# Kernel optimization log

Measured on AMD Instinct MI355X. Metric: run time of the kernel, lower is better.

The kernel has to match this reference:

```python
import jax, jax.numpy as jnp
import numpy as np

T, B, I, H = 2048, 64, 256, 256


def setup_inputs() -> dict:
    key = jax.random.key(0)
    ks = jax.random.split(key, 5)
    s = 1.0 / np.sqrt(H)
    return {
        "x": jax.random.normal(ks[0], (T, B, I), jnp.float32),
        "h0": jnp.zeros((B, H), jnp.float32),
        "c0": jnp.zeros((B, H), jnp.float32),
        "W_i": jax.random.uniform(ks[1], (4 * H, I), jnp.float32, -s, s),
        "W_h": jax.random.uniform(ks[2], (4 * H, H), jnp.float32, -s, s),
        "b_i": jax.random.uniform(ks[3], (4 * H,), jnp.float32, -s, s),
        "b_h": jax.random.uniform(ks[4], (4 * H,), jnp.float32, -s, s),
    }


def reference(x, h0, c0, W_i, W_h, b_i, b_h):
    # Precompute the input projection for all timesteps in one big GEMM:
    # [T,B,I] @ [I,4H] -> [T,B,4H]
    xproj = jnp.einsum("tbi,gi->tbg", x, W_i) + (b_i + b_h)

    def step(carry, xg):
        h, c = carry
        # subLSTM: all four gates are sigmoid. Gate order: in, out, z, forget.
        gates = jax.nn.sigmoid(xg + h @ W_h.T)  # [B,4H]
        i_g, o_g, z_g, f_g = jnp.split(gates, 4, axis=-1)
        c_new = c * f_g + z_g - i_g
        h_new = jax.nn.sigmoid(c_new) - o_g
        return (h_new, c_new), h_new

    (h_T, c_T), outputs = jax.lax.scan(step, (h0, c0), xproj)
    return outputs, (h_T, c_T)
```

## Files before the change

kernel.cpp:

```cpp
#include <hip/hip_runtime.h>


typedef __attribute__((ext_vector_type(4))) float f32x4;
typedef __attribute__((ext_vector_type(8))) short bf16x8;
typedef __attribute__((ext_vector_type(4))) int i32x4;
typedef __attribute__((ext_vector_type(4))) unsigned short u16x4;

constexpr float WSCALE = 2032.0f;
constexpr float SC = 1.0f / (2032.0f * 127.0f);

__device__ __forceinline__ unsigned short f2bf(float f) {
  unsigned u = __builtin_bit_cast(unsigned, f);
  u += 0x7fffu + ((u >> 16) & 1u);
  return (unsigned short)(u >> 16);
}
__device__ __forceinline__ float sigmf(float x) {
  return __builtin_amdgcn_rcpf(1.0f + __expf(-x));
}

__global__ void quantw_kernel(const float* __restrict__ Wh,
                              signed char* __restrict__ Wq) {
  int i = blockIdx.x * 256 + threadIdx.x;
  float q = rintf(Wh[i] * WSCALE);
  q = fminf(127.0f, fmaxf(-127.0f, q));
  Wq[i] = (signed char)(int)q;
}

__device__ __forceinline__ void gemm_body(char* smem, int gb,
                                          const float* __restrict__ x,
                                          const float* __restrict__ Wi,
                                          const float* __restrict__ bi,
                                          const float* __restrict__ bh,
                                          float* __restrict__ xpOut, long m0) {
  typedef unsigned short row72[72];
  row72* Al = (row72*)smem;
  row72* Bl = (row72*)(smem + 18432);
  const int tid = threadIdx.x;
  const int act = tid < 256;
  const int lane = tid & 63, wv = (tid >> 6) & 3;
  const int wm = wv >> 1, wn = wv & 1, cl = lane & 15, cg = lane >> 4;
  const int bx = gb >> 3, by = gb & 7;
  const long gm0 = m0 + (long)bx * 128;
  const int lm0 = bx * 128;
  const int n0 = by * 128;
  const int srow = (tid & 255) >> 1, sh = (tid & 1) * 32;

  f32x4 acc[4][4];
#pragma unroll
  for (int m = 0; m < 4; ++m)
#pragma unroll
    for (int n = 0; n < 4; ++n) acc[m][n] = (f32x4){0.f, 0.f, 0.f, 0.f};

  for (int kt = 0; kt < 4; ++kt) {
    if (act) {
      const float* pa = x + (gm0 + srow) * 256 + kt * 64 + sh;
      const float* pb = Wi + (long)(n0 + srow) * 256 + kt * 64 + sh;
#pragma unroll
      for (int j = 0; j < 8; ++j) {
        f32x4 va = *(const f32x4*)(pa + j * 4);
        f32x4 vb = *(const f32x4*)(pb + j * 4);
        u16x4 ua, ub;
#pragma unroll
        for (int k = 0; k < 4; ++k) { ua[k] = f2bf(va[k]); ub[k] = f2bf(vb[k]); }
        *(u16x4*)&Al[srow][sh + j * 4] = ua;
        *(u16x4*)&Bl[srow][sh + j * 4] = ub;
      }
    }
    __syncthreads();
    if (act) {
#pragma unroll
      for (int ks = 0; ks < 2; ++ks) {
        bf16x8 af[4], bfv[4];
#pragma unroll
        for (int m = 0; m < 4; ++m)
          af[m] = *(const bf16x8*)&Al[wm * 64 + m * 16 + cl][ks * 32 + cg * 8];
#pragma unroll
        for (int n = 0; n < 4; ++n)
          bfv[n] = *(const bf16x8*)&Bl[wn * 64 + n * 16 + cl][ks * 32 + cg * 8];
#pragma unroll
        for (int m = 0; m < 4; ++m)
#pragma unroll
          for (int n = 0; n < 4; ++n)
            acc[m][n] = __builtin_amdgcn_mfma_f32_16x16x32_bf16(
                af[m], bfv[n], acc[m][n], 0, 0, 0);
      }
    }
    __syncthreads();
  }
  if (act) {
#pragma unroll
    for (int n = 0; n < 4; ++n) {
      int gn = n0 + wn * 64 + n * 16 + cl;
      float bias = bi[gn] + bh[gn];
#pragma unroll
      for (int m = 0; m < 4; ++m) {
        int lrow = lm0 + wm * 64 + m * 16 + cg * 4;
#pragma unroll
        for (int r = 0; r < 4; ++r)
          xpOut[(long)(lrow + r) * 1024 + gn] = acc[m][n][r] + bias;
      }
    }
  }
}

#define SB() __builtin_amdgcn_sched_barrier(0)

#define RAW_BARRIER()                                         \
  do {                                                        \
    __builtin_amdgcn_sched_barrier(0);                        \
    asm volatile("s_waitcnt lgkmcnt(0)" ::: "memory");        \
    __builtin_amdgcn_s_barrier();                             \
    asm volatile("" ::: "memory");                            \
    __builtin_amdgcn_sched_barrier(0);                        \
  } while (0)

#define MFMA_PAIR16(P0_, P1_, Q0_, Q1_, TP, TQ)                               \
  asm volatile("s_setprio 1\n\t"                                              \
               "s_nop 3\n\t"                                                  \
               "v_mfma_i32_16x16x64_i8 %0, %20, %4, %24\n\t"                  \
               "v_mfma_i32_16x16x64_i8 %1, %20, %5, %24\n\t"                  \
               "v_mfma_i32_16x16x64_i8 %2, %20, %6, %24\n\t"                  \
               "v_mfma_i32_16x16x64_i8 %3, %20, %7, %24\n\t"                  \
               "v_mfma_i32_16x16x64_i8 %0, %21, %8, %0\n\t"                   \
               "v_mfma_i32_16x16x64_i8 %1, %21, %9, %1\n\t"                   \
               "v_mfma_i32_16x16x64_i8 %2, %21, %10, %2\n\t"                  \
               "v_mfma_i32_16x16x64_i8 %3, %21, %11, %3\n\t"                  \
               "v_mfma_i32_16x16x64_i8 %0, %22, %12, %0\n\t"                  \
               "v_mfma_i32_16x16x64_i8 %1, %22, %13, %1\n\t"                  \
               "v_mfma_i32_16x16x64_i8 %2, %22, %14, %2\n\t"                  \
               "v_mfma_i32_16x16x64_i8 %3, %22, %15, %3\n\t"                  \
               "v_mfma_i32_16x16x64_i8 %0, %23, %16, %0\n\t"                  \
               "v_mfma_i32_16x16x64_i8 %1, %23, %17, %1\n\t"                  \
               "v_mfma_i32_16x16x64_i8 %2, %23, %18, %2\n\t"                  \
               "v_mfma_i32_16x16x64_i8 %3, %23, %19, %3\n\t"                  \
               "s_setprio 0"                                                  \
               : "=&v"(P0_), "=&v"(P1_), "=&v"(Q0_), "=&v"(Q1_)               \
               : "a"(wf[TP][0][0]), "a"(wf[TP][1][0]), "a"(wf[TQ][0][0]),     \
                 "a"(wf[TQ][1][0]), "a"(wf[TP][0][1]), "a"(wf[TP][1][1]),     \
                 "a"(wf[TQ][0][1]), "a"(wf[TQ][1][1]), "a"(wf[TP][0][2]),     \
                 "a"(wf[TP][1][2]), "a"(wf[TQ][0][2]), "a"(wf[TQ][1][2]),     \
                 "a"(wf[TP][0][3]), "a"(wf[TP][1][3]), "a"(wf[TQ][0][3]),     \
                 "a"(wf[TQ][1][3]), "v"(bq0), "v"(bq1), "v"(bq2), "v"(bq3),   \
                 "v"(zq))

#define SEL1(A0_, A1_) (bsel_ ? (A1_)[0] : (A0_)[0])

#define BQ_AND_ACC(TT)                                                         \
    const int rs = (TT) & 1;                                                   \
    i32x4 bq0 = *(const i32x4*)((const char*)(&hq[rs][0]) + 0 + cg * 16);      \
    i32x4 bq1 = *(const i32x4*)((const char*)(&hq[rs][0]) + 64 + cg * 16);     \
    i32x4 bq2 = *(const i32x4*)((const char*)(&hq[rs][0]) + 128 + cg * 16);    \
    i32x4 bq3 = *(const i32x4*)((const char*)(&hq[rs][0]) + 192 + cg * 16);    \
    i32x4 a00, a01, a10, a11, a20, a21, a30, a31;

#define STEP_TAIL(TT)                                                          \
    float hv = sc_ - go;                                                       \
    int qv = (int)rintf(hv * 127.0f);                                          \
    if (lane < 32) {                                                           \
      ((signed char*)(&hq[rs ^ 1][0]))[u] = (signed char)qv;                   \
      out[((long)(t0 + (TT)) * 64 + b) * 256 + u] = hv;                        \
      if (last && (TT) == nt - 1) {                                            \
        out[33554432L + b * 256 + u] = hv;                                     \
        out[33554432L + 16384L + b * 256 + u] = c_own;                         \
      }                                                                        \
    }                                                                          \
    RAW_BARRIER();

#define STEP(TT, XBUF)                                                         \
  do {                                                                         \
    BQ_AND_ACC(TT)                                                             \
    MFMA_PAIR16(a00, a01, a10, a11, 0, 1);            \
    SB();                                                                      \
    float x3s_ = XBUF[3], x2s_ = XBUF[2], x1s_ = XBUF[1];                      \
    float gi = sigmf(XBUF[0] + SC * (float)SEL1(a00, a01));                    \
    SB();                                                                      \
    if ((TT) + 2 < nt) {       \
      _Pragma("unroll") for (int tg = 0; tg < 4; ++tg)                         \
          XBUF[tg] = xp[((long)((TT) + 2) * 64 + b) * 1024 + tg * 256 + u];    \
    } else {                                                                   \
      asm volatile("s_nop 7\n\ts_nop 7");                                      \
    }                                                                          \
    SB();                                                                      \
    float go = sigmf(x1s_ + SC * (float)SEL1(a10, a11));                       \
    SB();                                                                      \
    MFMA_PAIR16(a30, a31, a20, a21, 3, 2);                     \
    SB();                                                                      \
    float gf = sigmf(x3s_ + SC * (float)SEL1(a30, a31));                       \
    SB();                                                                      \
    float gz = sigmf(x2s_ + SC * (float)SEL1(a20, a21));                       \
    c_own = c_own * gf + gz - gi;                                              \
    float sc_ = sigmf(c_own);                                                  \
    STEP_TAIL(TT)                                                              \
  } while (0)

__device__ __forceinline__ void recur_body(
    char* smem, const float* __restrict__ xp, float* __restrict__ out,
    float* __restrict__ cst, int* __restrict__ hqst,
    const float* __restrict__ h0, const float* __restrict__ c0,
    const signed char* __restrict__ Wq, int t0, int nt, int first, int last) {
  const int b = blockIdx.x, tid = threadIdx.x;
  const int w = tid >> 6, lane = tid & 63, cl = lane & 15, cg = lane >> 4;
  const int bsel_ = cg & 1;
  const int u = w * 32 + bsel_ * 16 + cl;
  int(*hq)[64] = (int(*)[64])smem;

  i32x4 wf[4][2][4];
#pragma unroll
  for (int tg = 0; tg < 4; ++tg)
#pragma unroll
    for (int s = 0; s < 2; ++s)
#pragma unroll
      for (int q = 0; q < 4; ++q)
        wf[tg][s][q] = *(const i32x4*)(Wq +
                                       (tg * 256 + w * 32 + s * 16 + cl) * 256 +
                                       q * 64 + cg * 16);

  const i32x4 zq = {0, 0, 0, 0};

  float c_own = first ? c0[b * 256 + u] : cst[b * 256 + u];

  if (tid < 64) {
    int word;
    if (first) {
      int qj[4];
#pragma unroll
      for (int j = 0; j < 4; ++j) {
        float v = h0[b * 256 + tid * 4 + j];
        qj[j] = (int)rintf(fminf(1.0f, fmaxf(-1.0f, v)) * 127.0f);
      }
      word = (qj[0] & 255) | ((qj[1] & 255) << 8) | ((qj[2] & 255) << 16) |
             ((qj[3] & 255) << 24);
    } else {
      word = hqst[b * 64 + tid];
    }
    hq[0][tid] = word;
  }

  float xa[4], xb[4];
#pragma unroll
  for (int tg = 0; tg < 4; ++tg) {
    xa[tg] = xp[((long)0 * 64 + b) * 1024 + tg * 256 + u];
    xb[tg] = xp[((long)1 * 64 + b) * 1024 + tg * 256 + u];
  }
  __syncthreads();

  for (int t = 0; t < nt; t += 2) {
    STEP(t, xa);
    STEP(t + 1, xb);
  }

  if (lane < 32) cst[b * 256 + u] = c_own;
  if (tid < 64) hqst[b * 64 + tid] = hq[0][tid];
}

__global__ __launch_bounds__(512, 1) void fused_kernel(
    const float* __restrict__ x, const float* __restrict__ Wi,
    const float* __restrict__ bi, const float* __restrict__ bh,
    float* __restrict__ gslot, long m0, int have_gemm,
    const float* __restrict__ rslot, float* __restrict__ out,
    float* __restrict__ cst, int* __restrict__ hqst,
    const float* __restrict__ h0, const float* __restrict__ c0,
    const signed char* __restrict__ Wq, int t0, int nt, int first, int last,
    int have_recur) {
  __shared__ __align__(16) char smem[83968];
  if (blockIdx.x < 64) {
    if (have_recur)
      recur_body(smem, rslot, out, cst, hqst, h0, c0, Wq, t0, nt, first, last);
  } else {
    if (have_gemm) gemm_body(smem, blockIdx.x - 64, x, Wi, bi, bh, gslot, m0);
  }
}

extern "C" void kernel_launch(void* const* d_in, const int* in_sizes, int n_in,
                              void* d_out, int out_size, void* d_ws,
                              size_t ws_size, hipStream_t stream) {
  const float* x = (const float*)d_in[0];
  const float* h0 = (const float*)d_in[1];
  const float* c0 = (const float*)d_in[2];
  const float* Wi = (const float*)d_in[3];
  const float* Wh = (const float*)d_in[4];
  const float* bi = (const float*)d_in[5];
  const float* bh = (const float*)d_in[6];
  float* out = (float*)d_out;

  const size_t fixed = 262144  + 65536  + 16384 ;
  int chunkT = 32;
  const int cands[4] = {256, 128, 64, 32};
  for (int i = 0; i < 4; ++i) {
    size_t slot = (size_t)cands[i] * 64 * 1024 * 4;
    if (fixed + 2 * slot <= ws_size) { chunkT = cands[i]; break; }
  }

  char* p = (char*)d_ws;
  signed char* Wq = (signed char*)p;  p += 262144;
  float* cst = (float*)p;             p += 65536;
  int* hqst = (int*)p;                p += 16384;
  float* ring = (float*)p;
  const size_t slotElems = (size_t)chunkT * 64 * 1024;

  quantw_kernel<<<1024, 256, 0, stream>>>(Wh, Wq);

  const int nchunks = 2048 / chunkT;
  for (int c = 0; c <= nchunks; ++c) {
    const int hg = (c < nchunks) ? 1 : 0;
    const int hr = (c > 0) ? 1 : 0;
    float* gs = ring + (size_t)(c & 1) * slotElems;
    const float* rs = ring + (size_t)((c ^ 1) & 1) * slotElems;
    const int ngb = hg ? (chunkT / 2) * 8 : 0;
    fused_kernel<<<64 + ngb, 512, 0, stream>>>(
        x, Wi, bi, bh, gs, (long)c * chunkT * 64, hg, rs, out, cst, hqst, h0,
        c0, Wq, (c - 1) * chunkT, chunkT, (c == 1) ? 1 : 0,
        (c == nchunks) ? 1 : 0, hr);
  }
}
```

Baseline: 1.669 ms.

## Split recurrent step across 16 waves with one fused MFMA block per step

Each recurrence block now runs 1024 threads. Every wave owns 16 hidden units instead of 32, and each lane group keeps only a single 16-row weight fragment per gate. The two MFMA pair groups are merged into one 16-MFMA sequence that accumulates all four gates at once, which shortens the per-step dependency chain and lets all gate sigmoids run after a single matrix block. The cost is twice as many waves meeting at the per-step barrier. There is also the risk that the `launch_bounds(1024,4)` hint squeezes registers into spills, and the GEMM path now also launches with 1024 threads.

```diff
diff --git a/kernel.cpp b/kernel.cpp
--- a/kernel.cpp
+++ b/kernel.cpp
@@ -114,13 +114,13 @@
     __builtin_amdgcn_sched_barrier(0);                        \
   } while (0)
 
-#define MFMA_PAIR16(P0_, P1_, Q0_, Q1_, TP, TQ)                               \
+#define MFMA16(F_, Z_, I_, O_)                                                \
   asm volatile("s_setprio 1\n\t"                                              \
                "s_nop 3\n\t"                                                  \
-               "v_mfma_i32_16x16x64_i8 %0, %20, %4, %24\n\t"                  \
-               "v_mfma_i32_16x16x64_i8 %1, %20, %5, %24\n\t"                  \
-               "v_mfma_i32_16x16x64_i8 %2, %20, %6, %24\n\t"                  \
-               "v_mfma_i32_16x16x64_i8 %3, %20, %7, %24\n\t"                  \
+               "v_mfma_i32_16x16x64_i8 %0, %20, %4, %0\n\t"                   \
+               "v_mfma_i32_16x16x64_i8 %1, %20, %5, %1\n\t"                   \
+               "v_mfma_i32_16x16x64_i8 %2, %20, %6, %2\n\t"                   \
+               "v_mfma_i32_16x16x64_i8 %3, %20, %7, %3\n\t"                   \
                "v_mfma_i32_16x16x64_i8 %0, %21, %8, %0\n\t"                   \
                "v_mfma_i32_16x16x64_i8 %1, %21, %9, %1\n\t"                   \
                "v_mfma_i32_16x16x64_i8 %2, %21, %10, %2\n\t"                  \
@@ -133,30 +133,41 @@
                "v_mfma_i32_16x16x64_i8 %1, %23, %17, %1\n\t"                  \
                "v_mfma_i32_16x16x64_i8 %2, %23, %18, %2\n\t"                  \
                "v_mfma_i32_16x16x64_i8 %3, %23, %19, %3\n\t"                  \
-               "s_setprio 0"                                                  \
-               : "=&v"(P0_), "=&v"(P1_), "=&v"(Q0_), "=&v"(Q1_)               \
-               : "a"(wf[TP][0][0]), "a"(wf[TP][1][0]), "a"(wf[TQ][0][0]),     \
-                 "a"(wf[TQ][1][0]), "a"(wf[TP][0][1]), "a"(wf[TP][1][1]),     \
-                 "a"(wf[TQ][0][1]), "a"(wf[TQ][1][1]), "a"(wf[TP][0][2]),     \
-                 "a"(wf[TP][1][2]), "a"(wf[TQ][0][2]), "a"(wf[TQ][1][2]),     \
-                 "a"(wf[TP][0][3]), "a"(wf[TP][1][3]), "a"(wf[TQ][0][3]),     \
-                 "a"(wf[TQ][1][3]), "v"(bq0), "v"(bq1), "v"(bq2), "v"(bq3),   \
-                 "v"(zq))
-
-#define SEL1(A0_, A1_) (bsel_ ? (A1_)[0] : (A0_)[0])
-
-#define BQ_AND_ACC(TT)                                                         \
+               "s_setprio 0\n\t"                                              \
+               "s_nop 7\n\ts_nop 7"                                           \
+               : "+v"(F_), "+v"(Z_), "+v"(I_), "+v"(O_)                       \
+               : "a"(wf[3][0]), "a"(wf[2][0]), "a"(wf[0][0]), "a"(wf[1][0]),  \
+                 "a"(wf[3][1]), "a"(wf[2][1]), "a"(wf[0][1]), "a"(wf[1][1]),  \
+                 "a"(wf[3][2]), "a"(wf[2][2]), "a"(wf[0][2]), "a"(wf[1][2]),  \
+                 "a"(wf[3][3]), "a"(wf[2][3]), "a"(wf[0][3]), "a"(wf[1][3]),  \
+                 "v"(bq0), "v"(bq1), "v"(bq2), "v"(bq3))
+
+#define STEP(TT, XBUF)                                                         \
+  do {                                                                         \
     const int rs = (TT) & 1;                                                   \
     i32x4 bq0 = *(const i32x4*)((const char*)(&hq[rs][0]) + 0 + cg * 16);      \
     i32x4 bq1 = *(const i32x4*)((const char*)(&hq[rs][0]) + 64 + cg * 16);     \
     i32x4 bq2 = *(const i32x4*)((const char*)(&hq[rs][0]) + 128 + cg * 16);    \
     i32x4 bq3 = *(const i32x4*)((const char*)(&hq[rs][0]) + 192 + cg * 16);    \
-    i32x4 a00, a01, a10, a11, a20, a21, a30, a31;
-
-#define STEP_TAIL(TT)                                                          \
+    i32x4 aF = {0, 0, 0, 0}, aZ = {0, 0, 0, 0};                                \
+    i32x4 aI = {0, 0, 0, 0}, aO = {0, 0, 0, 0};                                \
+    MFMA16(aF, aZ, aI, aO);                                                    \
+    SB();                                                                      \
+    float x3s_ = XBUF[3], x2s_ = XBUF[2], x1s_ = XBUF[1], x0s_ = XBUF[0];      \
+    if ((TT) + 2 < nt) {                                                       \
+      _Pragma("unroll") for (int tg = 0; tg < 4; ++tg)                         \
+          XBUF[tg] = xp[((long)((TT) + 2) * 64 + b) * 1024 + tg * 256 + u];    \
+    }                                                                          \
+    SB();                                                                      \
+    float gf = sigmf(x3s_ + SC * (float)aF[0]);                                \
+    float gz = sigmf(x2s_ + SC * (float)aZ[0]);                                \
+    float gi = sigmf(x0s_ + SC * (float)aI[0]);                                \
+    c_own = c_own * gf + gz - gi;                                              \
+    float sc_ = sigmf(c_own);                                                  \
+    float go = sigmf(x1s_ + SC * (float)aO[0]);                                \
     float hv = sc_ - go;                                                       \
     int qv = (int)rintf(hv * 127.0f);                                          \
-    if (lane < 32) {                                                           \
+    if (cg0) {                                                                 \
       ((signed char*)(&hq[rs ^ 1][0]))[u] = (signed char)qv;                   \
       out[((long)(t0 + (TT)) * 64 + b) * 256 + u] = hv;                        \
       if (last && (TT) == nt - 1) {                                            \
@@ -164,33 +175,7 @@
         out[33554432L + 16384L + b * 256 + u] = c_own;                         \
       }                                                                        \
     }                                                                          \
-    RAW_BARRIER();
-
-#define STEP(TT, XBUF)                                                         \
-  do {                                                                         \
-    BQ_AND_ACC(TT)                                                             \
-    MFMA_PAIR16(a00, a01, a10, a11, 0, 1);            \
-    SB();                                                                      \
-    float x3s_ = XBUF[3], x2s_ = XBUF[2], x1s_ = XBUF[1];                      \
-    float gi = sigmf(XBUF[0] + SC * (float)SEL1(a00, a01));                    \
-    SB();                                                                      \
-    if ((TT) + 2 < nt) {       \
-      _Pragma("unroll") for (int tg = 0; tg < 4; ++tg)                         \
-          XBUF[tg] = xp[((long)((TT) + 2) * 64 + b) * 1024 + tg * 256 + u];    \
-    } else {                                                                   \
-      asm volatile("s_nop 7\n\ts_nop 7");                                      \
-    }                                                                          \
-    SB();                                                                      \
-    float go = sigmf(x1s_ + SC * (float)SEL1(a10, a11));                       \
-    SB();                                                                      \
-    MFMA_PAIR16(a30, a31, a20, a21, 3, 2);                     \
-    SB();                                                                      \
-    float gf = sigmf(x3s_ + SC * (float)SEL1(a30, a31));                       \
-    SB();                                                                      \
-    float gz = sigmf(x2s_ + SC * (float)SEL1(a20, a21));                       \
-    c_own = c_own * gf + gz - gi;                                              \
-    float sc_ = sigmf(c_own);                                                  \
-    STEP_TAIL(TT)                                                              \
+    RAW_BARRIER();                                                             \
   } while (0)
 
 __device__ __forceinline__ void recur_body(
@@ -200,22 +185,17 @@
     const signed char* __restrict__ Wq, int t0, int nt, int first, int last) {
   const int b = blockIdx.x, tid = threadIdx.x;
   const int w = tid >> 6, lane = tid & 63, cl = lane & 15, cg = lane >> 4;
-  const int bsel_ = cg & 1;
-  const int u = w * 32 + bsel_ * 16 + cl;
+  const int cg0 = (lane < 16);
+  const int u = w * 16 + cl;
   int(*hq)[64] = (int(*)[64])smem;
 
-  i32x4 wf[4][2][4];
+  i32x4 wf[4][4];
 #pragma unroll
   for (int tg = 0; tg < 4; ++tg)
 #pragma unroll
-    for (int s = 0; s < 2; ++s)
-#pragma unroll
-      for (int q = 0; q < 4; ++q)
-        wf[tg][s][q] = *(const i32x4*)(Wq +
-                                       (tg * 256 + w * 32 + s * 16 + cl) * 256 +
-                                       q * 64 + cg * 16);
-
-  const i32x4 zq = {0, 0, 0, 0};
+    for (int q = 0; q < 4; ++q)
+      wf[tg][q] = *(const i32x4*)(Wq + (tg * 256 + w * 16 + cl) * 256 +
+                                  q * 64 + cg * 16);
 
   float c_own = first ? c0[b * 256 + u] : cst[b * 256 + u];
 
@@ -249,11 +229,11 @@
     STEP(t + 1, xb);
   }
 
-  if (lane < 32) cst[b * 256 + u] = c_own;
+  if (cg0) cst[b * 256 + u] = c_own;
   if (tid < 64) hqst[b * 64 + tid] = hq[0][tid];
 }
 
-__global__ __launch_bounds__(512, 1) void fused_kernel(
+__global__ __launch_bounds__(1024, 4) void fused_kernel(
     const float* __restrict__ x, const float* __restrict__ Wi,
     const float* __restrict__ bi, const float* __restrict__ bh,
     float* __restrict__ gslot, long m0, int have_gemm,
@@ -307,7 +287,7 @@
     float* gs = ring + (size_t)(c & 1) * slotElems;
     const float* rs = ring + (size_t)((c ^ 1) & 1) * slotElems;
     const int ngb = hg ? (chunkT / 2) * 8 : 0;
-    fused_kernel<<<64 + ngb, 512, 0, stream>>>(
+    fused_kernel<<<64 + ngb, 1024, 0, stream>>>(
         x, Wi, bi, bh, gs, (long)c * chunkT * 64, hg, rs, out, cst, hqst, h0,
         c0, Wq, (c - 1) * chunkT, chunkT, (c == 1) ? 1 : 0,
         (c == nchunks) ? 1 : 0, hr);
```

Measured after the change: 1.757 ms. 5.3% more time.
